# Optimization experiments

Measured on AMD Instinct MI355X. Metric: run time of the kernel, lower is better.

The kernel has to match this reference:

```python
import jax, jax.numpy as jnp
import numpy as np

SYLL_V, WORD_V, K = 10000, 20000, 10
SYLL_D, WORD_D, H = 64, 32, 64  # H = hidden_dim // 2 per direction
B, T = 256, 512
IN_D = SYLL_D + WORD_D


def lstm_dir(x, w_ih, w_hh, b_ih, b_hh, reverse):
    # x: [B,T,D]; w_ih: [4H,D]; w_hh: [4H,H]; PyTorch gate order i,f,g,o
    b, t, _ = x.shape
    h = w_hh.shape[1]
    xp = jnp.einsum('btd,gd->btg', x, w_ih) + b_ih + b_hh  # [B,T,4H]
    if reverse:
        xp = xp[:, ::-1]
    def step(carry, xt):
        hs, cs = carry
        g = xt + hs @ w_hh.T
        i, f, gg, o = jnp.split(g, 4, axis=-1)
        i = jax.nn.sigmoid(i); f = jax.nn.sigmoid(f)
        gg = jnp.tanh(gg); o = jax.nn.sigmoid(o)
        cs = f * cs + i * gg
        hs = o * jnp.tanh(cs)
        return (hs, cs), hs
    h0 = jnp.zeros((b, h), x.dtype)
    _, hseq = jax.lax.scan(step, (h0, h0), jnp.swapaxes(xp, 0, 1))
    hseq = jnp.swapaxes(hseq, 0, 1)  # [B,T,H]
    if reverse:
        hseq = hseq[:, ::-1]
    return hseq


def crf_llh(emissions, tags, mask, start_t, end_t, trans):
    # torchcrf log-likelihood, batch_first. emissions [B,T,K], tags [B,T], mask [B,T] bool
    b, t, k = emissions.shape
    mf = mask.astype(emissions.dtype)
    ar = jnp.arange(b)
    # numerator: score of the given tag path
    num = start_t[tags[:, 0]] + emissions[ar, 0, tags[:, 0]]
    e_tag = jnp.take_along_axis(emissions, tags[:, :, None], axis=2)[:, :, 0]  # [B,T]
    tr = trans[tags[:, :-1], tags[:, 1:]]  # [B,T-1]
    num = num + jnp.sum(mf[:, 1:] * (tr + e_tag[:, 1:]), axis=1)
    seq_len = jnp.sum(mask.astype(jnp.int32), axis=1)
    last_tags = jnp.take_along_axis(tags, (seq_len - 1)[:, None], axis=1)[:, 0]
    num = num + end_t[last_tags]
    # denominator: log partition via forward algorithm (sequential logsumexp scan)
    alpha0 = start_t[None, :] + emissions[:, 0]  # [B,K]
    def step(alpha, inp):
        em_t, m_t = inp  # [B,K], [B]
        nxt = jax.nn.logsumexp(alpha[:, :, None] + trans[None] + em_t[:, None, :], axis=1)
        return jnp.where(m_t[:, None], nxt, alpha), None
    alpha, _ = jax.lax.scan(
        step, alpha0,
        (jnp.swapaxes(emissions[:, 1:], 0, 1), jnp.swapaxes(mask[:, 1:], 0, 1)))
    den = jax.nn.logsumexp(alpha + end_t[None, :], axis=1)
    return num - den


def setup_inputs() -> dict:
    key = jax.random.key(0)
    ks = jax.random.split(key, 20)
    s = 0.1
    syll_emb = jax.random.normal(ks[0], (SYLL_V, SYLL_D), jnp.float32) * s
    syll_emb = syll_emb.at[0].set(0.0)  # padding_idx
    word_emb = jax.random.normal(ks[1], (WORD_V, WORD_D), jnp.float32) * s
    word_emb = word_emb.at[0].set(0.0)
    def lstm_params(i):
        return (jax.random.normal(ks[i], (4 * H, IN_D), jnp.float32) * s,
                jax.random.normal(ks[i + 1], (4 * H, H), jnp.float32) * s,
                jax.random.normal(ks[i + 2], (4 * H,), jnp.float32) * s,
                jax.random.normal(ks[i + 3], (4 * H,), jnp.float32) * s)
    w_ih_f, w_hh_f, b_ih_f, b_hh_f = lstm_params(2)
    w_ih_b, w_hh_b, b_ih_b, b_hh_b = lstm_params(6)
    W_tag = jax.random.normal(ks[10], (K, 2 * H), jnp.float32) * s
    b_tag = jax.random.normal(ks[11], (K,), jnp.float32) * s
    crf_start = jax.random.normal(ks[12], (K,), jnp.float32) * s
    crf_end = jax.random.normal(ks[13], (K,), jnp.float32) * s
    crf_trans = jax.random.normal(ks[14], (K, K), jnp.float32) * s
    return {
        'syll_input': jax.random.randint(ks[15], (B, T), 0, SYLL_V),
        'word_input': jax.random.randint(ks[16], (B, T), 0, WORD_V),
        'tags': jax.random.randint(ks[17], (B, T), 0, K),
        'mask': jnp.ones((B, T), jnp.bool_),
        'syll_emb': syll_emb, 'word_emb': word_emb,
        'w_ih_f': w_ih_f, 'w_hh_f': w_hh_f, 'b_ih_f': b_ih_f, 'b_hh_f': b_hh_f,
        'w_ih_b': w_ih_b, 'w_hh_b': w_hh_b, 'b_ih_b': b_ih_b, 'b_hh_b': b_hh_b,
        'W_tag': W_tag, 'b_tag': b_tag,
        'crf_start': crf_start, 'crf_end': crf_end, 'crf_trans': crf_trans,
    }


def reference(syll_input, word_input, tags, mask,
              syll_emb, word_emb,
              w_ih_f, w_hh_f, b_ih_f, b_hh_f,
              w_ih_b, w_hh_b, b_ih_b, b_hh_b,
              W_tag, b_tag, crf_start, crf_end, crf_trans):
    combined = jnp.concatenate([syll_emb[syll_input], word_emb[word_input]], axis=2)  # [B,T,96]
    h_f = lstm_dir(combined, w_ih_f, w_hh_f, b_ih_f, b_hh_f, reverse=False)
    h_b = lstm_dir(combined, w_ih_b, w_hh_b, b_ih_b, b_hh_b, reverse=True)
    lstm_out = jnp.concatenate([h_f, h_b], axis=2)  # [B,T,128]
    emissions = jnp.einsum('bth,kh->btk', lstm_out, W_tag) + b_tag
    llh = crf_llh(emissions, tags, mask, crf_start, crf_end, crf_trans)
    return -jnp.mean(llh)  # reduction='mean', negated
```

## Files before the change

### kernel.cpp

```cpp
#include <hip/hip_runtime.h>

typedef unsigned short ushort_t;
typedef unsigned int uint_t;
typedef __attribute__((ext_vector_type(8))) short short8;
typedef __attribute__((ext_vector_type(4))) float f32x4;
typedef __fp16 fp16x2 __attribute__((ext_vector_type(2)));

#define B_SZ 256
#define T_LEN 512
#define Hd 64
#define KT 10
#define XP_RB 128

#define L2E  1.4426950408889634f
#define L2E2 2.8853900817779268f

#define F_EM 0
#define F_OMEGA (F_EM + B_SZ*T_LEN*KT)
#define F_S1 (F_OMEGA + B_SZ*64*100)
#define F_XP (F_S1 + B_SZ*64)
#define F_HSEQ (F_XP + (2*B_SZ*T_LEN*256)/2)
#define F_WBUF (F_HSEQ + (B_SZ*T_LEN*2*Hd)/2)
#define F_BIAS (F_WBUF + 49152)

template <int V> struct ic { static constexpr int v = V; };

__device__ __forceinline__ ushort_t f2bf(float f) {
    uint_t u = __float_as_uint(f);
    uint_t r = (u + 0x7FFFu + ((u >> 16) & 1u)) >> 16;
    return (ushort_t)r;
}
__device__ __forceinline__ float f16f(uint_t u) {
    ushort_t us = (ushort_t)u;
    _Float16 h = *(_Float16*)&us;
    return (float)h;
}
__device__ __forceinline__ short8 cvt8(const float* p) {
    float4 x0 = *(const float4*)&p[0];
    float4 x1 = *(const float4*)&p[4];
    short8 f;
    f[0] = (short)f2bf(x0.x); f[1] = (short)f2bf(x0.y);
    f[2] = (short)f2bf(x0.z); f[3] = (short)f2bf(x0.w);
    f[4] = (short)f2bf(x1.x); f[5] = (short)f2bf(x1.y);
    f[6] = (short)f2bf(x1.z); f[7] = (short)f2bf(x1.w);
    return f;
}
__device__ __forceinline__ short8 cvt8s(const float* p, float sc) {
    float4 x0 = *(const float4*)&p[0];
    float4 x1 = *(const float4*)&p[4];
    short8 f;
    f[0] = (short)f2bf(x0.x*sc); f[1] = (short)f2bf(x0.y*sc);
    f[2] = (short)f2bf(x0.z*sc); f[3] = (short)f2bf(x0.w*sc);
    f[4] = (short)f2bf(x1.x*sc); f[5] = (short)f2bf(x1.y*sc);
    f[6] = (short)f2bf(x1.z*sc); f[7] = (short)f2bf(x1.w*sc);
    return f;
}

__global__ __launch_bounds__(256) void wprep_kernel(
    const float* __restrict__ w_ih_f, const float* __restrict__ w_ih_b,
    const float* __restrict__ b_ih_f, const float* __restrict__ b_hh_f,
    const float* __restrict__ b_ih_b, const float* __restrict__ b_hh_b,
    short8* __restrict__ wbuf, float* __restrict__ biasbuf)
{
    const int dir = blockIdx.x;
    const float* __restrict__ wih = dir ? w_ih_b : w_ih_f;
    const float* __restrict__ bi = dir ? b_ih_b : b_ih_f;
    const float* __restrict__ bh = dir ? b_hh_b : b_hh_f;
    const int tid = threadIdx.x;
    const int w = tid >> 6;
    const int l = tid & 63;
    const int rg = l >> 4;
    const int c = l & 15;

    {
        int s = tid;
        int g = 64 * (s & 3) + (s >> 2);
        float gsc = ((s & 3) == 2) ? L2E2 : -L2E;
        biasbuf[dir * 256 + s] = 0.5f * (bi[g] + bh[g]) * gsc;
    }
#pragma unroll
    for (int mt = 0; mt < 4; mt++) {
        int s = 64 * w + 16 * mt + c;
        int g = 64 * (s & 3) + (s >> 2);
        float gsc = ((s & 3) == 2) ? L2E2 : -L2E;
#pragma unroll
        for (int ch = 0; ch < 3; ch++) {
            const float* wp = &wih[g * 96 + ch * 32 + rg * 8];
            float4 x0 = *(const float4*)&wp[0];
            float4 x1 = *(const float4*)&wp[4];
            float vv[8] = {x0.x, x0.y, x0.z, x0.w, x1.x, x1.y, x1.z, x1.w};
            short8 h8, l8;
#pragma unroll
            for (int j = 0; j < 8; j++) {
                float sv = vv[j] * gsc;
                ushort_t hb2 = f2bf(sv);
                h8[j] = (short)hb2;
                l8[j] = (short)f2bf(sv - __uint_as_float((uint_t)hb2 << 16));
            }
            int base = (((dir * 4 + w) * 4 + mt) * 3 + ch) * 2;
            wbuf[(size_t)(base + 0) * 64 + l] = h8;
            wbuf[(size_t)(base + 1) * 64 + l] = l8;
        }
    }
}

__global__ __launch_bounds__(256) void xp_kernel(
    const int* __restrict__ syll, const int* __restrict__ word,
    const float* __restrict__ syll_emb, const float* __restrict__ word_emb,
    const short8* __restrict__ wbuf, const float* __restrict__ biasbuf,
    ushort_t* __restrict__ xp)
{
    const int nrb = (B_SZ * T_LEN) / XP_RB;
    const int rb = blockIdx.x & (nrb - 1);
    const int dir = blockIdx.x >> 10;
    const int m0 = rb * XP_RB;
    const int b = m0 >> 9;
    const int t0 = m0 & (T_LEN - 1);

    const int tid = threadIdx.x;
    const int w = tid >> 6;
    const int l = tid & 63;
    const int rg = l >> 4;
    const int c = l & 15;

    __shared__ int six[XP_RB], wix[XP_RB];
    __shared__ __align__(16) ushort_t Xh[XP_RB][104];

    if (tid < XP_RB) six[tid] = syll[b * T_LEN + t0 + tid];
    else wix[tid - XP_RB] = word[b * T_LEN + t0 + tid - XP_RB];
    __syncthreads();
    for (int i = tid; i < XP_RB * 96; i += 256) {
        int row = i / 96, k = i - row * 96;
        float v = (k < 64) ? syll_emb[six[row] * 64 + k]
                           : word_emb[wix[row] * 32 + (k - 64)];
        Xh[row][k] = f2bf(v);
    }
    __syncthreads();

    const size_t obase = ((size_t)(dir * B_SZ + b) * T_LEN + t0) * 256;
#pragma unroll
    for (int mt = 0; mt < 4; mt++) {
        short8 Ah[3], Al[3];
#pragma unroll
        for (int ch = 0; ch < 3; ch++) {
            int base = (((dir * 4 + w) * 4 + mt) * 3 + ch) * 2;
            Ah[ch] = wbuf[(size_t)(base + 0) * 64 + l];
            Al[ch] = wbuf[(size_t)(base + 1) * 64 + l];
        }
        const f32x4 bias = *(const f32x4*)&biasbuf[dir * 256 + 64 * w + 16 * mt + 4 * rg];
        for (int nt = 0; nt < XP_RB / 16; nt++) {
            short8 Bh_[3];
#pragma unroll
            for (int ch = 0; ch < 3; ch++)
                Bh_[ch] = *(const short8*)&Xh[nt * 16 + c][ch * 32 + rg * 8];
            f32x4 acc = bias;
#pragma unroll
            for (int ch = 0; ch < 3; ch++) {
                acc = __builtin_amdgcn_mfma_f32_16x16x32_bf16(Ah[ch], Bh_[ch], acc, 0, 0, 0);
                acc = __builtin_amdgcn_mfma_f32_16x16x32_bf16(Al[ch], Bh_[ch], acc, 0, 0, 0);
            }
            fp16x2 p0 = __builtin_amdgcn_cvt_pkrtz(acc[0], acc[1]);
            fp16x2 p1 = __builtin_amdgcn_cvt_pkrtz(acc[2], acc[3]);
            uint2 o;
            o.x = *(uint_t*)&p0;
            o.y = *(uint_t*)&p1;
            *(uint2*)&xp[obase + (size_t)(nt * 16 + c) * 256 + 64 * w + 16 * mt + 4 * rg] = o;
        }
    }
}

__global__ __launch_bounds__(256, 1) void lstm_kernel(
    const float* __restrict__ w_hh_f, const float* __restrict__ w_hh_b,
    const ushort_t* __restrict__ xp, ushort_t* __restrict__ h_out)
{
    const int dir = blockIdx.x & 1;
    const int bA = (blockIdx.x >> 1) * 4;
    const int tid = threadIdx.x;
    const int w = tid >> 6;
    const int l = tid & 63;
    const int rg = l >> 4;
    const int c = l & 15;
    const int cell = 16 * w + c;

    const float* __restrict__ whh = dir ? w_hh_b : w_hh_f;

    short8 bfrag[4][2];
#pragma unroll
    for (int tau = 0; tau < 4; tau++) {
        const float sc = (tau == 2) ? L2E2 : -L2E;
#pragma unroll
        for (int chk = 0; chk < 2; chk++)
            bfrag[tau][chk] = cvt8s(whh + (size_t)(64 * tau + cell) * Hd + chk * 32 + rg * 8, sc);
    }

    __shared__ __align__(16) ushort_t h_lds[2][16][72];
    for (int i = tid; i < 2 * 16 * 72; i += 256) ((ushort_t*)h_lds)[i] = 0;

    const int chain = bA + rg;
    const int p0 = dir ? (T_LEN - 1) : 0;
    const int st = dir ? -256 : 256;
    const ushort_t* xq = xp + ((size_t)(dir * B_SZ + chain) * T_LEN + p0) * 256 + cell * 4;
    uint2 xb[4];
#pragma unroll
    for (int j = 0; j < 4; j++) xb[j] = *(const uint2*)(xq + j * st);
    const ushort_t* pf = xq + 4 * st;

    float cst = 0.f;
    ushort_t* hp = h_out + ((size_t)(chain * T_LEN + p0) * 2 + dir) * Hd + cell;
    const int hstep = dir ? -128 : 128;
    const f32x4 zro = {0.f, 0.f, 0.f, 0.f};
    __syncthreads();

    auto step = [&](auto STC, int t) {
        constexpr int ST = decltype(STC)::v;
        uint_t lo_u = xb[ST].x, hi_u = xb[ST].y;
        float ps0 = f16f(lo_u & 0xffffu);
        float ps1 = f16f(lo_u >> 16);
        float ps2 = f16f(hi_u & 0xffffu);
        float ps3 = f16f(hi_u >> 16);
        xb[ST] = *(const uint2*)pf;
        pf += st;

        f32x4 cc0 = {ps0, 0.f, 0.f, 0.f};
        f32x4 cc1 = {ps1, 0.f, 0.f, 0.f};
        f32x4 cc2 = {ps2, 0.f, 0.f, 0.f};
        f32x4 cc3 = {ps3, 0.f, 0.f, 0.f};
        const ushort_t* hrow = &h_lds[t & 1][c][0];
        short8 a0 = *(const short8*)(hrow + rg * 8);
        short8 a1 = *(const short8*)(hrow + 32 + rg * 8);
        f32x4 p00 = __builtin_amdgcn_mfma_f32_16x16x32_bf16(a0, bfrag[0][0], cc0, 0, 0, 0);
        f32x4 p10 = __builtin_amdgcn_mfma_f32_16x16x32_bf16(a0, bfrag[1][0], cc1, 0, 0, 0);
        f32x4 p20 = __builtin_amdgcn_mfma_f32_16x16x32_bf16(a0, bfrag[2][0], cc2, 0, 0, 0);
        f32x4 p30 = __builtin_amdgcn_mfma_f32_16x16x32_bf16(a0, bfrag[3][0], cc3, 0, 0, 0);
        f32x4 p01 = __builtin_amdgcn_mfma_f32_16x16x32_bf16(a1, bfrag[0][1], zro, 0, 0, 0);
        f32x4 p11 = __builtin_amdgcn_mfma_f32_16x16x32_bf16(a1, bfrag[1][1], zro, 0, 0, 0);
        f32x4 p21 = __builtin_amdgcn_mfma_f32_16x16x32_bf16(a1, bfrag[2][1], zro, 0, 0, 0);
        f32x4 p31 = __builtin_amdgcn_mfma_f32_16x16x32_bf16(a1, bfrag[3][1], zro, 0, 0, 0);

        float ai = p00[0] + p01[0];
        float af = p10[0] + p11[0];
        float ag = fminf(p20[0] + p21[0], 60.0f);
        float ao = p30[0] + p31[0];
        float ei = __builtin_amdgcn_exp2f(ai);
        float ef = __builtin_amdgcn_exp2f(af);
        float Eg = __builtin_amdgcn_exp2f(ag);
        float eo = __builtin_amdgcn_exp2f(ao);
        float e3 = 1.0f + ef;
        float pe = (1.0f + ei) * (1.0f + Eg);
        float num = __builtin_fmaf(Eg - 1.0f, e3, cst * pe);
        float cn = num * __builtin_amdgcn_rcpf(e3 * pe);
        cst = cn;
        float t2 = fminf(cn * L2E2, 60.0f);
        float E2 = __builtin_amdgcn_exp2f(t2);
        float h = (E2 - 1.0f) * __builtin_amdgcn_rcpf((1.0f + eo) * (1.0f + E2));

        ushort_t hb = f2bf(h);
        h_lds[(t + 1) & 1][4 * rg][cell] = hb;
        *hp = hb;
        hp += hstep;
        __builtin_amdgcn_sched_barrier(0);
        asm volatile("s_waitcnt lgkmcnt(0)" ::: "memory");
        __builtin_amdgcn_s_barrier();
        __builtin_amdgcn_sched_barrier(0);
    };

    for (int t = 0; t < T_LEN; t += 4) {
        step(ic<0>{}, t);
        step(ic<1>{}, t + 1);
        step(ic<2>{}, t + 2);
        step(ic<3>{}, t + 3);
    }
}

#define EMIS_G 4
__global__ __launch_bounds__(64) void emis_kernel(
    const ushort_t* __restrict__ hseq, const float* __restrict__ W_tag,
    const float* __restrict__ b_tag, float* __restrict__ em)
{
    const int l = threadIdx.x;
    const int rg = l >> 4;
    const int n = l & 15;

    short8 bf[4];
#pragma unroll
    for (int ch = 0; ch < 4; ch++) {
        if (n < KT) bf[ch] = cvt8(W_tag + (size_t)n * 128 + ch * 32 + rg * 8);
        else { short8 z = {0,0,0,0,0,0,0,0}; bf[ch] = z; }
    }
    const float btv = (n < KT) ? b_tag[n] : 0.f;

#pragma unroll
    for (int gi = 0; gi < EMIS_G; gi++) {
        const int row0 = (blockIdx.x * EMIS_G + gi) * 16;
        const ushort_t* __restrict__ ar = hseq + (size_t)(row0 + n) * 128 + rg * 8;
        short8 a0 = *(const short8*)&ar[0];
        short8 a1 = *(const short8*)&ar[32];
        short8 a2 = *(const short8*)&ar[64];
        short8 a3 = *(const short8*)&ar[96];
        f32x4 acc = {btv, btv, btv, btv};
        acc = __builtin_amdgcn_mfma_f32_16x16x32_bf16(a0, bf[0], acc, 0, 0, 0);
        acc = __builtin_amdgcn_mfma_f32_16x16x32_bf16(a1, bf[1], acc, 0, 0, 0);
        acc = __builtin_amdgcn_mfma_f32_16x16x32_bf16(a2, bf[2], acc, 0, 0, 0);
        acc = __builtin_amdgcn_mfma_f32_16x16x32_bf16(a3, bf[3], acc, 0, 0, 0);
        if (n < KT) {
#pragma unroll
            for (int r = 0; r < 4; r++)
                em[(size_t)(row0 + 4 * rg + r) * KT + n] = acc[r];
        }
    }
}

__global__ __launch_bounds__(64) void crf_stage1(
    const float* __restrict__ em, const float* __restrict__ trans,
    float* __restrict__ Omega, float* __restrict__ S1)
{
    __shared__ float etT[KT * 12];
    const int tid = threadIdx.x;
    for (int i = tid; i < KT * 12; i += 64) etT[i] = 0.f;
    __syncthreads();
    for (int i = tid; i < 100; i += 64) {
        int jj = i / 10, k = i % 10;
        etT[k * 12 + jj] = __expf(trans[i]);
    }
    __syncthreads();

    const int id = blockIdx.x * 64 + tid;
    const int b = id >> 6, c = id & 63;
    const int t0 = (c == 0) ? 1 : c * 8;
    const int nt = (c == 0) ? 7 : 8;

    float run[10][10];
    float s = 0.f;

    float ecur[10];
    {
        const float* r = em + (size_t)(b * T_LEN + t0) * KT;
#pragma unroll
        for (int k = 0; k < 10; k++) ecur[k] = r[k];
    }
    {
        float mx = ecur[0];
#pragma unroll
        for (int k = 1; k < 10; k++) mx = fmaxf(mx, ecur[k]);
        s += mx;
        float ee[10];
#pragma unroll
        for (int k = 0; k < 10; k++) ee[k] = __expf(ecur[k] - mx);
#pragma unroll
        for (int jj = 0; jj < 10; jj++)
#pragma unroll
            for (int k = 0; k < 10; k++) run[jj][k] = etT[k * 12 + jj] * ee[k];
    }
    float enx[10];
    if (nt > 1) {
        const float* r = em + (size_t)(b * T_LEN + t0 + 1) * KT;
#pragma unroll
        for (int k = 0; k < 10; k++) enx[k] = r[k];
    }
    for (int li = 1; li < nt; li++) {
        float mx = enx[0];
#pragma unroll
        for (int k = 1; k < 10; k++) mx = fmaxf(mx, enx[k]);
        s += mx;
        float ee[10];
#pragma unroll
        for (int k = 0; k < 10; k++) ee[k] = __expf(enx[k] - mx);
        if (li + 1 < nt) {
            const float* r = em + (size_t)(b * T_LEN + t0 + li + 1) * KT;
#pragma unroll
            for (int k = 0; k < 10; k++) enx[k] = r[k];
        }
#pragma unroll
        for (int i = 0; i < 10; i++) {
            float outp[10];
#pragma unroll
            for (int k = 0; k < 10; k++) {
                float sum = 0.f;
#pragma unroll
                for (int jj = 0; jj < 10; jj++) sum += run[i][jj] * etT[k * 12 + jj];
                outp[k] = sum * ee[k];
            }
#pragma unroll
            for (int k = 0; k < 10; k++) run[i][k] = outp[k];
        }
    }
    float m = run[0][0];
#pragma unroll
    for (int i = 0; i < 10; i++)
#pragma unroll
        for (int k = 0; k < 10; k++) m = fmaxf(m, run[i][k]);
    float inv = 1.0f / m;
    s += __logf(m);
#pragma unroll
    for (int i = 0; i < 10; i++)
#pragma unroll
        for (int k = 0; k < 10; k++) Omega[(size_t)id * 100 + i * 10 + k] = run[i][k] * inv;
    S1[id] = s;
}

__global__ __launch_bounds__(256) void crf_stage2(
    const float* __restrict__ Omega, const float* __restrict__ S1,
    const float* __restrict__ em, const int* __restrict__ tags,
    const float* __restrict__ start_t, const float* __restrict__ end_t,
    const float* __restrict__ trans, float* __restrict__ out)
{
    const int b = blockIdx.x;
    const int tid = threadIdx.x;
    __shared__ float bufA[64 * 120];
    __shared__ float bufB[32 * 120];
    __shared__ float sh_red[4];
    __shared__ float sh_s;
    __shared__ float scl_sh[32];
    __shared__ float lg_sh[32];
    __shared__ float lg_acc_sh;

    for (int idx = tid; idx < 6400; idx += 256) {
        int c = idx / 100, e = idx % 100;
        bufA[c * 120 + (e / 10) * 12 + (e % 10)] = Omega[(size_t)(b * 64 + c) * 100 + e];
    }
    if (tid < 64) {
        float v = S1[b * 64 + tid];
        for (int off = 32; off; off >>= 1) v += __shfl_down(v, off);
        if (tid == 0) sh_s = v;
    }
    if (tid == 0) lg_acc_sh = 0.f;
    __syncthreads();

    float* src = bufA;
    float* dst = bufB;
    for (int n = 32; n >= 1; n >>= 1) {
        for (int idx = tid; idx < n * 100; idx += 256) {
            int p = idx / 100, e = idx % 100, i = e / 10, k = e % 10;
            const float* A = src + (2 * p) * 120;
            const float* Bm = src + (2 * p + 1) * 120;
            float sum = 0.f;
#pragma unroll
            for (int jj = 0; jj < 10; jj++) sum += A[i * 12 + jj] * Bm[jj * 12 + k];
            dst[p * 120 + i * 12 + k] = sum;
        }
        __syncthreads();
        if (tid < n) {
            const float* M = dst + tid * 120;
            float mx = 0.f;
            for (int i = 0; i < 10; i++)
                for (int k = 0; k < 10; k++) mx = fmaxf(mx, M[i * 12 + k]);
            scl_sh[tid] = 1.0f / mx;
            lg_sh[tid] = __logf(mx);
        }
        __syncthreads();
        if (tid == 0) {
            float s = 0.f;
            for (int p = 0; p < n; p++) s += lg_sh[p];
            lg_acc_sh += s;
        }
        for (int idx = tid; idx < n * 100; idx += 256) {
            int p = idx / 100, e = idx % 100;
            dst[p * 120 + (e / 10) * 12 + (e % 10)] *= scl_sh[p];
        }
        __syncthreads();
        float* t_ = src; src = dst; dst = t_;
    }

    float den = 0.f;
    if (tid < 64) {
        float val = 0.f;
        float mx0 = 0.f;
        if (tid < 10) {
            mx0 = -1e30f;
            for (int jj = 0; jj < 10; jj++) mx0 = fmaxf(mx0, start_t[jj] + em[(size_t)(b * T_LEN) * KT + jj]);
            for (int jj = 0; jj < 10; jj++) {
                float v0 = __expf(start_t[jj] + em[(size_t)(b * T_LEN) * KT + jj] - mx0);
                val += v0 * src[jj * 12 + tid];
            }
            val *= __expf(end_t[tid]);
        }
        for (int off = 8; off; off >>= 1) val += __shfl_down(val, off);
        if (tid == 0) den = __logf(val) + mx0 + sh_s + lg_acc_sh;
    }

    float part = 0.f;
    const int* __restrict__ tg = tags + b * T_LEN;
    for (int t = tid; t < T_LEN; t += 256) {
        int cur = tg[t];
        if (t == 0) part += start_t[cur] + em[(size_t)(b * T_LEN) * KT + cur];
        else part += trans[tg[t - 1] * KT + cur] + em[(size_t)(b * T_LEN + t) * KT + cur];
        if (t == T_LEN - 1) part += end_t[cur];
    }
    for (int off = 32; off; off >>= 1) part += __shfl_down(part, off);
    if ((tid & 63) == 0) sh_red[tid >> 6] = part;
    __syncthreads();
    if (tid == 0) {
        float num = sh_red[0] + sh_red[1] + sh_red[2] + sh_red[3];
        float llh = num - den;
        atomicAdd(out, llh * (-1.0f / 256.0f));
    }
}

extern "C" void kernel_launch(void* const* d_in, const int* in_sizes, int n_in,
                              void* d_out, int out_size, void* d_ws, size_t ws_size,
                              hipStream_t stream) {
    const int* syll      = (const int*)d_in[0];
    const int* word      = (const int*)d_in[1];
    const int* tags      = (const int*)d_in[2];
    const float* syll_emb = (const float*)d_in[4];
    const float* word_emb = (const float*)d_in[5];
    const float* w_ih_f  = (const float*)d_in[6];
    const float* w_hh_f  = (const float*)d_in[7];
    const float* b_ih_f  = (const float*)d_in[8];
    const float* b_hh_f  = (const float*)d_in[9];
    const float* w_ih_b  = (const float*)d_in[10];
    const float* w_hh_b  = (const float*)d_in[11];
    const float* b_ih_b  = (const float*)d_in[12];
    const float* b_hh_b  = (const float*)d_in[13];
    const float* W_tag   = (const float*)d_in[14];
    const float* b_tag   = (const float*)d_in[15];
    const float* crf_start = (const float*)d_in[16];
    const float* crf_end   = (const float*)d_in[17];
    const float* crf_trans = (const float*)d_in[18];

    float* out = (float*)d_out;
    float* ws = (float*)d_ws;
    ushort_t* xp = (ushort_t*)(ws + F_XP);
    ushort_t* hseq = (ushort_t*)(ws + F_HSEQ);
    short8* wbuf = (short8*)(ws + F_WBUF);
    float* biasbuf = ws + F_BIAS;

    hipMemsetAsync(d_out, 0, sizeof(float), stream);

    wprep_kernel<<<2, 256, 0, stream>>>(
        w_ih_f, w_ih_b, b_ih_f, b_hh_f, b_ih_b, b_hh_b, wbuf, biasbuf);

    xp_kernel<<<2 * (B_SZ * T_LEN / XP_RB), 256, 0, stream>>>(
        syll, word, syll_emb, word_emb, wbuf, biasbuf, xp);

    lstm_kernel<<<B_SZ * 2 / 4, 256, 0, stream>>>(
        w_hh_f, w_hh_b, xp, hseq);

    emis_kernel<<<B_SZ * T_LEN / (16 * EMIS_G), 64, 0, stream>>>(
        hseq, W_tag, b_tag, ws + F_EM);

    crf_stage1<<<256, 64, 0, stream>>>(ws + F_EM, crf_trans, ws + F_OMEGA, ws + F_S1);

    crf_stage2<<<B_SZ, 256, 0, stream>>>(
        ws + F_OMEGA, ws + F_S1, ws + F_EM, tags, crf_start, crf_end, crf_trans, out);
}
```

Baseline: 352.5 us.

## Fuse emission projection into LSTM recurrence, drop hidden-sequence buffer and emis kernel

Each LSTM step now runs two extra MFMAs that multiply the current hidden state by its direction's half of W_tag, and writes per-direction partial emissions (padded to 16) instead of storing the bf16 hidden sequence. The separate emission kernel is removed, and the CRF stages sum forward and backward partials plus the tag bias when they read emissions. This avoids writing and re-reading the hidden sequence and saves one launch. In exchange it adds work to the latency-bound serial step and doubles the emission reads in the CRF stages.

```diff
diff --git a/kernel.cpp b/kernel.cpp
--- a/kernel.cpp
+++ b/kernel.cpp
@@ -15,12 +15,12 @@
 #define L2E  1.4426950408889634f
 #define L2E2 2.8853900817779268f
 
-#define F_EM 0
-#define F_OMEGA (F_EM + B_SZ*T_LEN*KT)
+#define F_EMF 0
+#define F_EMB (F_EMF + B_SZ*T_LEN*16)
+#define F_OMEGA (F_EMB + B_SZ*T_LEN*16)
 #define F_S1 (F_OMEGA + B_SZ*64*100)
 #define F_XP (F_S1 + B_SZ*64)
-#define F_HSEQ (F_XP + (2*B_SZ*T_LEN*256)/2)
-#define F_WBUF (F_HSEQ + (B_SZ*T_LEN*2*Hd)/2)
+#define F_WBUF (F_XP + (2*B_SZ*T_LEN*256)/2)
 #define F_BIAS (F_WBUF + 49152)
 
 template <int V> struct ic { static constexpr int v = V; };
@@ -171,7 +171,9 @@
 
 __global__ __launch_bounds__(256, 1) void lstm_kernel(
     const float* __restrict__ w_hh_f, const float* __restrict__ w_hh_b,
-    const ushort_t* __restrict__ xp, ushort_t* __restrict__ h_out)
+    const float* __restrict__ W_tag,
+    const ushort_t* __restrict__ xp, float* __restrict__ emF,
+    float* __restrict__ emB)
 {
     const int dir = blockIdx.x & 1;
     const int bA = (blockIdx.x >> 1) * 4;
@@ -192,6 +194,12 @@
         for (int chk = 0; chk < 2; chk++)
             bfrag[tau][chk] = cvt8s(whh + (size_t)(64 * tau + cell) * Hd + chk * 32 + rg * 8, sc);
     }
+    short8 tfrag[2];
+#pragma unroll
+    for (int chk = 0; chk < 2; chk++) {
+        if (c < KT) tfrag[chk] = cvt8(W_tag + (size_t)c * 128 + dir * 64 + chk * 32 + rg * 8);
+        else { short8 z = {0,0,0,0,0,0,0,0}; tfrag[chk] = z; }
+    }
 
     __shared__ __align__(16) ushort_t h_lds[2][16][72];
     for (int i = tid; i < 2 * 16 * 72; i += 256) ((ushort_t*)h_lds)[i] = 0;
@@ -206,13 +214,20 @@
     const ushort_t* pf = xq + 4 * st;
 
     float cst = 0.f;
-    ushort_t* hp = h_out + ((size_t)(chain * T_LEN + p0) * 2 + dir) * Hd + cell;
-    const int hstep = dir ? -128 : 128;
+    float* __restrict__ emX = dir ? emB : emF;
+    float* ep = emX + ((size_t)((bA + rg) * T_LEN + p0)) * 16 + c;
+    const int estep = dir ? -16 : 16;
+    const bool emlane = (w == 0) && (c < KT);
+
     const f32x4 zro = {0.f, 0.f, 0.f, 0.f};
     __syncthreads();
 
     auto step = [&](auto STC, int t) {
         constexpr int ST = decltype(STC)::v;
+        const ushort_t* hrow = &h_lds[t & 1][c][0];
+        short8 a0 = *(const short8*)(hrow + rg * 8);
+        short8 a1 = *(const short8*)(hrow + 32 + rg * 8);
+
         uint_t lo_u = xb[ST].x, hi_u = xb[ST].y;
         float ps0 = f16f(lo_u & 0xffffu);
         float ps1 = f16f(lo_u >> 16);
@@ -225,9 +240,6 @@
         f32x4 cc1 = {ps1, 0.f, 0.f, 0.f};
         f32x4 cc2 = {ps2, 0.f, 0.f, 0.f};
         f32x4 cc3 = {ps3, 0.f, 0.f, 0.f};
-        const ushort_t* hrow = &h_lds[t & 1][c][0];
-        short8 a0 = *(const short8*)(hrow + rg * 8);
-        short8 a1 = *(const short8*)(hrow + 32 + rg * 8);
         f32x4 p00 = __builtin_amdgcn_mfma_f32_16x16x32_bf16(a0, bfrag[0][0], cc0, 0, 0, 0);
         f32x4 p10 = __builtin_amdgcn_mfma_f32_16x16x32_bf16(a0, bfrag[1][0], cc1, 0, 0, 0);
         f32x4 p20 = __builtin_amdgcn_mfma_f32_16x16x32_bf16(a0, bfrag[2][0], cc2, 0, 0, 0);
@@ -236,6 +248,8 @@
         f32x4 p11 = __builtin_amdgcn_mfma_f32_16x16x32_bf16(a1, bfrag[1][1], zro, 0, 0, 0);
         f32x4 p21 = __builtin_amdgcn_mfma_f32_16x16x32_bf16(a1, bfrag[2][1], zro, 0, 0, 0);
         f32x4 p31 = __builtin_amdgcn_mfma_f32_16x16x32_bf16(a1, bfrag[3][1], zro, 0, 0, 0);
+        f32x4 emacc = __builtin_amdgcn_mfma_f32_16x16x32_bf16(a0, tfrag[0], zro, 0, 0, 0);
+        emacc = __builtin_amdgcn_mfma_f32_16x16x32_bf16(a1, tfrag[1], emacc, 0, 0, 0);
 
         float ai = p00[0] + p01[0];
         float af = p10[0] + p11[0];
@@ -254,10 +268,13 @@
         float E2 = __builtin_amdgcn_exp2f(t2);
         float h = (E2 - 1.0f) * __builtin_amdgcn_rcpf((1.0f + eo) * (1.0f + E2));
 
+        if (t > 0) {
+            if (emlane) *ep = emacc[0];
+            ep += estep;
+        }
+
         ushort_t hb = f2bf(h);
         h_lds[(t + 1) & 1][4 * rg][cell] = hb;
-        *hp = hb;
-        hp += hstep;
         __builtin_amdgcn_sched_barrier(0);
         asm volatile("s_waitcnt lgkmcnt(0)" ::: "memory");
         __builtin_amdgcn_s_barrier();
@@ -270,48 +287,19 @@
         step(ic<2>{}, t + 2);
         step(ic<3>{}, t + 3);
     }
-}
-
-#define EMIS_G 4
-__global__ __launch_bounds__(64) void emis_kernel(
-    const ushort_t* __restrict__ hseq, const float* __restrict__ W_tag,
-    const float* __restrict__ b_tag, float* __restrict__ em)
-{
-    const int l = threadIdx.x;
-    const int rg = l >> 4;
-    const int n = l & 15;
-
-    short8 bf[4];
-#pragma unroll
-    for (int ch = 0; ch < 4; ch++) {
-        if (n < KT) bf[ch] = cvt8(W_tag + (size_t)n * 128 + ch * 32 + rg * 8);
-        else { short8 z = {0,0,0,0,0,0,0,0}; bf[ch] = z; }
-    }
-    const float btv = (n < KT) ? b_tag[n] : 0.f;
-
-#pragma unroll
-    for (int gi = 0; gi < EMIS_G; gi++) {
-        const int row0 = (blockIdx.x * EMIS_G + gi) * 16;
-        const ushort_t* __restrict__ ar = hseq + (size_t)(row0 + n) * 128 + rg * 8;
-        short8 a0 = *(const short8*)&ar[0];
-        short8 a1 = *(const short8*)&ar[32];
-        short8 a2 = *(const short8*)&ar[64];
-        short8 a3 = *(const short8*)&ar[96];
-        f32x4 acc = {btv, btv, btv, btv};
-        acc = __builtin_amdgcn_mfma_f32_16x16x32_bf16(a0, bf[0], acc, 0, 0, 0);
-        acc = __builtin_amdgcn_mfma_f32_16x16x32_bf16(a1, bf[1], acc, 0, 0, 0);
-        acc = __builtin_amdgcn_mfma_f32_16x16x32_bf16(a2, bf[2], acc, 0, 0, 0);
-        acc = __builtin_amdgcn_mfma_f32_16x16x32_bf16(a3, bf[3], acc, 0, 0, 0);
-        if (n < KT) {
-#pragma unroll
-            for (int r = 0; r < 4; r++)
-                em[(size_t)(row0 + 4 * rg + r) * KT + n] = acc[r];
-        }
+    {
+        const ushort_t* hrow = &h_lds[0][c][0];
+        short8 a0 = *(const short8*)(hrow + rg * 8);
+        short8 a1 = *(const short8*)(hrow + 32 + rg * 8);
+        f32x4 emacc = __builtin_amdgcn_mfma_f32_16x16x32_bf16(a0, tfrag[0], zro, 0, 0, 0);
+        emacc = __builtin_amdgcn_mfma_f32_16x16x32_bf16(a1, tfrag[1], emacc, 0, 0, 0);
+        if (emlane) *ep = emacc[0];
     }
 }
 
 __global__ __launch_bounds__(64) void crf_stage1(
-    const float* __restrict__ em, const float* __restrict__ trans,
+    const float* __restrict__ emF, const float* __restrict__ emB,
+    const float* __restrict__ b_tag, const float* __restrict__ trans,
     float* __restrict__ Omega, float* __restrict__ S1)
 {
     __shared__ float etT[KT * 12];
@@ -324,6 +312,10 @@
     }
     __syncthreads();
 
+    float btg[10];
+#pragma unroll
+    for (int k = 0; k < 10; k++) btg[k] = b_tag[k];
+
     const int id = blockIdx.x * 64 + tid;
     const int b = id >> 6, c = id & 63;
     const int t0 = (c == 0) ? 1 : c * 8;
@@ -334,9 +326,10 @@
 
     float ecur[10];
     {
-        const float* r = em + (size_t)(b * T_LEN + t0) * KT;
-#pragma unroll
-        for (int k = 0; k < 10; k++) ecur[k] = r[k];
+        const float* rF = emF + (size_t)(b * T_LEN + t0) * 16;
+        const float* rB = emB + (size_t)(b * T_LEN + t0) * 16;
+#pragma unroll
+        for (int k = 0; k < 10; k++) ecur[k] = rF[k] + rB[k] + btg[k];
     }
     {
         float mx = ecur[0];
@@ -353,9 +346,10 @@
     }
     float enx[10];
     if (nt > 1) {
-        const float* r = em + (size_t)(b * T_LEN + t0 + 1) * KT;
-#pragma unroll
-        for (int k = 0; k < 10; k++) enx[k] = r[k];
+        const float* rF = emF + (size_t)(b * T_LEN + t0 + 1) * 16;
+        const float* rB = emB + (size_t)(b * T_LEN + t0 + 1) * 16;
+#pragma unroll
+        for (int k = 0; k < 10; k++) enx[k] = rF[k] + rB[k] + btg[k];
     }
     for (int li = 1; li < nt; li++) {
         float mx = enx[0];
@@ -366,9 +360,10 @@
 #pragma unroll
         for (int k = 0; k < 10; k++) ee[k] = __expf(enx[k] - mx);
         if (li + 1 < nt) {
-            const float* r = em + (size_t)(b * T_LEN + t0 + li + 1) * KT;
-#pragma unroll
-            for (int k = 0; k < 10; k++) enx[k] = r[k];
+            const float* rF = emF + (size_t)(b * T_LEN + t0 + li + 1) * 16;
+            const float* rB = emB + (size_t)(b * T_LEN + t0 + li + 1) * 16;
+#pragma unroll
+            for (int k = 0; k < 10; k++) enx[k] = rF[k] + rB[k] + btg[k];
         }
 #pragma unroll
         for (int i = 0; i < 10; i++) {
@@ -400,7 +395,8 @@
 
 __global__ __launch_bounds__(256) void crf_stage2(
     const float* __restrict__ Omega, const float* __restrict__ S1,
-    const float* __restrict__ em, const int* __restrict__ tags,
+    const float* __restrict__ emF, const float* __restrict__ emB,
+    const float* __restrict__ b_tag, const int* __restrict__ tags,
     const float* __restrict__ start_t, const float* __restrict__ end_t,
     const float* __restrict__ trans, float* __restrict__ out)
 {
@@ -467,9 +463,13 @@
         float mx0 = 0.f;
         if (tid < 10) {
             mx0 = -1e30f;
-            for (int jj = 0; jj < 10; jj++) mx0 = fmaxf(mx0, start_t[jj] + em[(size_t)(b * T_LEN) * KT + jj]);
             for (int jj = 0; jj < 10; jj++) {
-                float v0 = __expf(start_t[jj] + em[(size_t)(b * T_LEN) * KT + jj] - mx0);
+                float e0 = emF[(size_t)(b * T_LEN) * 16 + jj] + emB[(size_t)(b * T_LEN) * 16 + jj] + b_tag[jj];
+                mx0 = fmaxf(mx0, start_t[jj] + e0);
+            }
+            for (int jj = 0; jj < 10; jj++) {
+                float e0 = emF[(size_t)(b * T_LEN) * 16 + jj] + emB[(size_t)(b * T_LEN) * 16 + jj] + b_tag[jj];
+                float v0 = __expf(start_t[jj] + e0 - mx0);
                 val += v0 * src[jj * 12 + tid];
             }
             val *= __expf(end_t[tid]);
@@ -482,8 +482,9 @@
     const int* __restrict__ tg = tags + b * T_LEN;
     for (int t = tid; t < T_LEN; t += 256) {
         int cur = tg[t];
-        if (t == 0) part += start_t[cur] + em[(size_t)(b * T_LEN) * KT + cur];
-        else part += trans[tg[t - 1] * KT + cur] + em[(size_t)(b * T_LEN + t) * KT + cur];
+        float ev = emF[(size_t)(b * T_LEN + t) * 16 + cur] + emB[(size_t)(b * T_LEN + t) * 16 + cur] + b_tag[cur];
+        if (t == 0) part += start_t[cur] + ev;
+        else part += trans[tg[t - 1] * KT + cur] + ev;
         if (t == T_LEN - 1) part += end_t[cur];
     }
     for (int off = 32; off; off >>= 1) part += __shfl_down(part, off);
@@ -520,8 +521,9 @@
 
     float* out = (float*)d_out;
     float* ws = (float*)d_ws;
+    float* emF = ws + F_EMF;
+    float* emB = ws + F_EMB;
     ushort_t* xp = (ushort_t*)(ws + F_XP);
-    ushort_t* hseq = (ushort_t*)(ws + F_HSEQ);
     short8* wbuf = (short8*)(ws + F_WBUF);
     float* biasbuf = ws + F_BIAS;
 
@@ -534,13 +536,10 @@
         syll, word, syll_emb, word_emb, wbuf, biasbuf, xp);
 
     lstm_kernel<<<B_SZ * 2 / 4, 256, 0, stream>>>(
-        w_hh_f, w_hh_b, xp, hseq);
-
-    emis_kernel<<<B_SZ * T_LEN / (16 * EMIS_G), 64, 0, stream>>>(
-        hseq, W_tag, b_tag, ws + F_EM);
-
-    crf_stage1<<<256, 64, 0, stream>>>(ws + F_EM, crf_trans, ws + F_OMEGA, ws + F_S1);
+        w_hh_f, w_hh_b, W_tag, xp, emF, emB);
+
+    crf_stage1<<<256, 64, 0, stream>>>(emF, emB, b_tag, crf_trans, ws + F_OMEGA, ws + F_S1);
 
     crf_stage2<<<B_SZ, 256, 0, stream>>>(
-        ws + F_OMEGA, ws + F_S1, ws + F_EM, tags, crf_start, crf_end, crf_trans, out);
-}
+        ws + F_OMEGA, ws + F_S1, emF, emB, b_tag, tags, crf_start, crf_end, crf_trans, out);
+}
```

After: 399.0 us. 1.13x slower.
